# Optimization experiments

Measured on AMD Instinct MI355X. Metric: run time of the kernel, lower is better.

## Reference

```python
import jax, jax.numpy as jnp
import numpy as np

B, T, HID = 4, 2048, 2048
N_HEAD, N_KV, HD = 16, 2, 128
N_REP = N_HEAD // N_KV


def setup_inputs() -> dict:
    key = jax.random.key(0)
    ks = jax.random.split(key, 7)
    s = 0.02
    return {
        "x": jax.random.normal(ks[0], (B, T, HID), jnp.float32),
        "cos": jax.random.normal(ks[1], (T, 1, HD // 2), jnp.float32),
        "sin": jax.random.normal(ks[2], (T, 1, HD // 2), jnp.float32),
        "Wq": jax.random.normal(ks[3], (N_HEAD * HD, HID), jnp.float32) * s,
        "Wk": jax.random.normal(ks[4], (N_KV * HD, HID), jnp.float32) * s,
        "Wv": jax.random.normal(ks[5], (N_KV * HD, HID), jnp.float32) * s,
        "Wo": jax.random.normal(ks[6], (HID, HID), jnp.float32) * s,
    }


def _rope(x, cos, sin):
    # x: (B, T, H, HD); cos/sin: (T, 1, HD//2) broadcast over B and H
    x_r = x[..., 0::2]
    x_i = x[..., 1::2]
    out_r = x_r * cos - x_i * sin
    out_i = x_r * sin + x_i * cos
    return jnp.stack([out_r, out_i], axis=-1).reshape(x.shape)


def _rms_norm(x):
    eps = jnp.finfo(x.dtype).eps
    var = jnp.mean(jnp.square(x), axis=-1, keepdims=True)
    return x * jax.lax.rsqrt(var + eps)


def reference(x, cos, sin, Wq, Wk, Wv, Wo):
    b, t, _ = x.shape
    q = (x @ Wq.T).reshape(b, t, N_HEAD, HD)
    k = (x @ Wk.T).reshape(b, t, N_KV, HD)
    v = (x @ Wv.T).reshape(b, t, N_KV, HD)
    q = _rms_norm(_rope(q, cos, sin))
    k = _rms_norm(_rope(k, cos, sin))
    # GQA without materializing repeated K/V: group q heads per kv head
    # q: (b, t, n_kv, n_rep, hd) -> (b, n_kv, n_rep, t, hd)
    q = q.reshape(b, t, N_KV, N_REP, HD).transpose(0, 2, 3, 1, 4)
    k = k.transpose(0, 2, 1, 3)  # (b, n_kv, t, hd)
    v = v.transpose(0, 2, 1, 3)
    scale = 1.0 / jnp.sqrt(jnp.asarray(HD, x.dtype))
    scores = jnp.einsum("bgrtd,bgsd->bgrts", q, k) * scale
    causal = jnp.tril(jnp.ones((t, t), dtype=bool))
    scores = jnp.where(causal, scores, jnp.asarray(-jnp.inf, scores.dtype))
    attn = jax.nn.softmax(scores, axis=-1)
    y = jnp.einsum("bgrts,bgsd->bgrtd", attn, v)
    # (b, n_kv, n_rep, t, hd) -> (b, t, n_head*hd)
    y = y.transpose(0, 3, 1, 2, 4).reshape(b, t, N_HEAD * HD)
    return y @ Wo.T
```

## Files before the change

### kernel.cpp

```cpp
#include <hip/hip_runtime.h>

#define B_    4
#define T_    2048
#define HID_  2048
#define NH_   16
#define NKV_  2
#define HD_   128
#define M_    (B_ * T_)
#define NQKV_ 2560

typedef __bf16 bf16x8 __attribute__((ext_vector_type(8)));
typedef float  f32x4  __attribute__((ext_vector_type(4)));

#define AS1 __attribute__((address_space(1)))
#define AS3 __attribute__((address_space(3)))

#if __has_builtin(__builtin_amdgcn_exp2f)
#define EXP2(x) __builtin_amdgcn_exp2f(x)
#else
#define EXP2(x) exp2f(x)
#endif

__device__ __forceinline__ void load_lds16(const void* g, void* l) {
  __builtin_amdgcn_global_load_lds((const AS1 unsigned int*)g,
                                   (AS3 unsigned int*)l, 16, 0, 0);
}

__device__ __forceinline__ unsigned short f2bf(float x) {
  union { float f; unsigned u; } a; a.f = x;
  unsigned r = a.u + 0x7fffu + ((a.u >> 16) & 1u);
  return (unsigned short)(r >> 16);
}
__device__ __forceinline__ float bf2f(unsigned h) {
  union { unsigned u; float f; } a; a.u = h << 16;
  return a.f;
}
__device__ __forceinline__ unsigned pk_rtz(float lo, float hi) {
  union { float f; unsigned u; } a, b; a.f = lo; b.f = hi;
  return (a.u >> 16) | (b.u & 0xffff0000u);
}

__global__ __launch_bounds__(256) void cast_bf16(const float* __restrict__ in,
                                                 unsigned short* __restrict__ out,
                                                 int n4) {
  int i = blockIdx.x * 256 + threadIdx.x;
  if (i >= n4) return;
  float4 v = ((const float4*)in)[i];
  ushort4 o;
  o.x = f2bf(v.x); o.y = f2bf(v.y); o.z = f2bf(v.z); o.w = f2bf(v.w);
  ((ushort4*)out)[i] = o;
}

__global__ __launch_bounds__(256) void cast_w(const float* __restrict__ Wq,
                                              const float* __restrict__ Wk,
                                              const float* __restrict__ Wv,
                                              unsigned short* __restrict__ out) {
  int i = blockIdx.x * 256 + threadIdx.x;
  const float* src; int j;
  if (i < 1048576)      { src = Wq; j = i; }
  else if (i < 1179648) { src = Wk; j = i - 1048576; }
  else                  { src = Wv; j = i - 1179648; }
  float4 v = ((const float4*)src)[j];
  ushort4 o;
  o.x = f2bf(v.x); o.y = f2bf(v.y); o.z = f2bf(v.z); o.w = f2bf(v.w);
  ((ushort4*)out)[i] = o;
}

template <int OUT_BF16>
__global__ __launch_bounds__(256) void gemm_bt(const unsigned short* __restrict__ A,
                                               const unsigned short* __restrict__ Bm,
                                               void* __restrict__ C,
                                               int M, int N, int K) {
  __shared__ __align__(16) unsigned short As[128 * 32];
  __shared__ __align__(16) unsigned short Bs[128 * 32];
  const int tid = threadIdx.x;
  const int w = tid >> 6, lane = tid & 63;
  const int m0 = blockIdx.y << 7, n0 = blockIdx.x << 7;
  const int c = lane & 15, grp = lane >> 4;
  const int lr = lane >> 2;
  const int su = (((lane & 3) ^ ((lr >> 1) & 3)) << 3);
  const int sw = (c >> 1) & 3;
  const int wm = (w & 1) << 6, wn = (w >> 1) << 6;
  f32x4 acc[4][4] = {};
  for (int k0 = 0; k0 < K; k0 += 32) {
    __syncthreads();
    {
      int r0 = w << 4;
      load_lds16(A + (size_t)(m0 + r0 + lr) * K + k0 + su, &As[r0 * 32]);
      load_lds16(A + (size_t)(m0 + 64 + r0 + lr) * K + k0 + su, &As[(64 + r0) * 32]);
      load_lds16(Bm + (size_t)(n0 + r0 + lr) * K + k0 + su, &Bs[r0 * 32]);
      load_lds16(Bm + (size_t)(n0 + 64 + r0 + lr) * K + k0 + su, &Bs[(64 + r0) * 32]);
    }
    __syncthreads();
    bf16x8 af[4], bf[4];
#pragma unroll
    for (int i = 0; i < 4; i++)
      af[i] = *(const bf16x8*)&As[(wm + i * 16 + c) * 32 + ((grp ^ sw) << 3)];
#pragma unroll
    for (int j = 0; j < 4; j++)
      bf[j] = *(const bf16x8*)&Bs[(wn + j * 16 + c) * 32 + ((grp ^ sw) << 3)];
#pragma unroll
    for (int i = 0; i < 4; i++)
#pragma unroll
      for (int j = 0; j < 4; j++)
        acc[i][j] = __builtin_amdgcn_mfma_f32_16x16x32_bf16(af[i], bf[j], acc[i][j], 0, 0, 0);
  }
#pragma unroll
  for (int i = 0; i < 4; i++)
#pragma unroll
    for (int j = 0; j < 4; j++)
#pragma unroll
      for (int r = 0; r < 4; r++) {
        int row = m0 + wm + i * 16 + grp * 4 + r;
        int col = n0 + wn + j * 16 + c;
        float v = acc[i][j][r];
        if (OUT_BF16) ((unsigned short*)C)[(size_t)row * N + col] = f2bf(v);
        else          ((float*)C)[(size_t)row * N + col] = v;
      }
}

__global__ __launch_bounds__(256) void rope_norm(const unsigned short* __restrict__ qkv,
                                                 const float* __restrict__ cosb,
                                                 const float* __restrict__ sinb,
                                                 unsigned short* __restrict__ qo,
                                                 unsigned short* __restrict__ ko,
                                                 unsigned short* __restrict__ vo) {
  const int m = blockIdx.x;
  const int b = m >> 11, t = m & 2047;
  const int w = threadIdx.x >> 6, lane = threadIdx.x & 63;
  const float cv = cosb[t * 64 + lane], sv = sinb[t * 64 + lane];
  const unsigned short* row = qkv + (size_t)m * NQKV_;
  const float QSCL = 0.08838834764831845f * 1.4426950408889634f;
  for (int hh = w; hh < 20; hh += 4) {
    if (hh < 18) {
      const int col0 = (hh < 16) ? hh * 128 : 2048 + (hh - 16) * 128;
      unsigned pr = *(const unsigned*)(row + col0 + 2 * lane);
      float xr = bf2f(pr & 0xffffu), xi = bf2f(pr >> 16);
      float orr = xr * cv - xi * sv;
      float oi  = xr * sv + xi * cv;
      float ss = orr * orr + oi * oi;
#pragma unroll
      for (int off = 1; off < 64; off <<= 1) ss += __shfl_xor(ss, off);
      float scl = rsqrtf(ss * (1.0f / 128.0f) + 1.1920929e-07f);
      if (hh < 16) {
        float s2 = scl * QSCL;
        unsigned out = (unsigned)f2bf(orr * s2) | ((unsigned)f2bf(oi * s2) << 16);
        *(unsigned*)(qo + (((size_t)(b * NH_ + hh)) * T_ + t) * HD_ + 2 * lane) = out;
      } else {
        unsigned out = (unsigned)f2bf(orr * scl) | ((unsigned)f2bf(oi * scl) << 16);
        *(unsigned*)(ko + (((size_t)(b * NKV_ + (hh - 16))) * T_ + t) * HD_ + 2 * lane) = out;
      }
    } else {
      const int gg = hh - 18;
      unsigned pr = *(const unsigned*)(row + 2304 + gg * 128 + 2 * lane);
      *(unsigned*)(vo + (((size_t)(b * NKV_ + gg)) * T_ + t) * HD_ + 2 * lane) = pr;
    }
  }
}

__global__ __launch_bounds__(256) void transpose_v(const unsigned short* __restrict__ v,
                                                   unsigned short* __restrict__ vt) {
  __shared__ unsigned short tile[64][65];
  const int bg = blockIdx.z;
  const int t0 = blockIdx.x << 6, h0 = blockIdx.y << 6;
  const unsigned short* src = v + (size_t)bg * T_ * HD_;
  unsigned short* dst = vt + (size_t)bg * T_ * HD_;
  const int tid = threadIdx.x;
  const int rr = tid >> 4, cc = (tid & 15) << 2;
  const int u = (cc >> 2) & 7;
  const int cp = (cc & 32) + 16 * (u & 1) + 4 * ((u >> 1) & 3);
#pragma unroll
  for (int it = 0; it < 4; it++) {
    int r = rr + it * 16;
    ushort4 d = *(const ushort4*)(src + (size_t)(t0 + r) * HD_ + h0 + cc);
    tile[r][cc + 0] = d.x; tile[r][cc + 1] = d.y;
    tile[r][cc + 2] = d.z; tile[r][cc + 3] = d.w;
  }
  __syncthreads();
#pragma unroll
  for (int it = 0; it < 4; it++) {
    int r = rr + it * 16;
    ushort4 d;
    d.x = tile[cp + 0][r]; d.y = tile[cp + 1][r];
    d.z = tile[cp + 2][r]; d.w = tile[cp + 3][r];
    *(ushort4*)(dst + (size_t)(h0 + r) * T_ + t0 + cc) = d;
  }
}

__global__ __launch_bounds__(256, 2) void flash_attn(const unsigned short* __restrict__ q,
                                                     const unsigned short* __restrict__ k,
                                                     const unsigned short* __restrict__ vt,
                                                     unsigned short* __restrict__ y) {
  __shared__ __align__(16) unsigned short Kb[2][8192];
  __shared__ __align__(16) unsigned short Vb[2][8192];
  const int tid = threadIdx.x;
  const int w = tid >> 6, lane = tid & 63;
  const int c = lane & 15, grp = lane >> 4;
  const int lr = lane >> 2;
  const int sw = (c >> 1) & 3;
  const int su = (((lane & 3) ^ ((lr >> 1) & 3)) << 3);
  const int t0 = (15 - (int)blockIdx.x) << 7;
  const int t0w = t0 + w * 32;
  const int hq = blockIdx.y, b = blockIdx.z, g = hq >> 3;
  const unsigned short* qbase = q + (((size_t)(b * NH_ + hq)) * T_ + t0) * HD_;
  const unsigned short* kbase = k + ((size_t)(b * NKV_ + g)) * T_ * HD_;
  const unsigned short* vtbase = vt + ((size_t)(b * NKV_ + g)) * HD_ * T_;

  bf16x8 qf[2][4];
#pragma unroll
  for (int ti = 0; ti < 2; ti++)
#pragma unroll
    for (int ks = 0; ks < 4; ks++)
      qf[ti][ks] = *(const bf16x8*)(qbase + (size_t)(w * 32 + ti * 16 + c) * HD_ + ks * 32 + grp * 8);

  f32x4 oacc[2][8] = {};
  float mrun[2], lrun[2];
  mrun[0] = mrun[1] = -__builtin_inff();
  lrun[0] = lrun[1] = 0.f;

  auto stage = [&](int s0, int bb) {
    const unsigned short* kp = kbase + (size_t)(s0 + w * 16 + lr) * HD_ + su;
#pragma unroll
    for (int dc = 0; dc < 4; dc++)
      load_lds16(kp + dc * 32, &Kb[bb][dc * 2048 + (w * 16) * 32]);
    const unsigned short* vp = vtbase + s0 + su;
#pragma unroll
    for (int ks = 0; ks < 2; ks++)
#pragma unroll
      for (int jj = 0; jj < 2; jj++)
        load_lds16(vp + (size_t)(w * 32 + jj * 16 + lr) * T_ + ks * 32,
                   &Vb[bb][ks * 4096 + (w * 32 + jj * 16) * 32]);
  };

  const int nch = (t0 >> 6) + 2;
  stage(0, 0);
  __syncthreads();
  for (int ic = 0; ic < nch; ic++) {
    const int s0 = ic << 6, bb = ic & 1;
    if (ic + 1 < nch) stage((ic + 1) << 6, bb ^ 1);
    if (s0 <= t0w + 31) {
      const unsigned short* Kc = Kb[bb];
      const unsigned short* Vc = Vb[bb];
      f32x4 st[2][4] = {};
#pragma unroll
      for (int s = 0; s < 4; s++)
#pragma unroll
        for (int kvt = 0; kvt < 4; kvt++) {
          bf16x8 ak = *(const bf16x8*)&Kc[s * 2048 + (kvt * 16 + c) * 32 + ((grp ^ sw) << 3)];
          st[0][kvt] = __builtin_amdgcn_mfma_f32_16x16x32_bf16(ak, qf[0][s], st[0][kvt], 0, 0, 0);
          st[1][kvt] = __builtin_amdgcn_mfma_f32_16x16x32_bf16(ak, qf[1][s], st[1][kvt], 0, 0, 0);
        }
      if (s0 + 63 > t0w) {
#pragma unroll
        for (int ti = 0; ti < 2; ti++)
#pragma unroll
          for (int kvt = 0; kvt < 4; kvt++)
#pragma unroll
            for (int r = 0; r < 4; r++) {
              int kv = s0 + kvt * 16 + grp * 4 + r;
              int qq = t0w + ti * 16 + c;
              if (kv > qq) st[ti][kvt][r] = -__builtin_inff();
            }
      }
      unsigned pkv[2][4][2];
#pragma unroll
      for (int ti = 0; ti < 2; ti++) {
        float rm = st[ti][0][0];
#pragma unroll
        for (int kvt = 0; kvt < 4; kvt++)
#pragma unroll
          for (int r = 0; r < 4; r++) rm = fmaxf(rm, st[ti][kvt][r]);
        rm = fmaxf(rm, __shfl_xor(rm, 16));
        rm = fmaxf(rm, __shfl_xor(rm, 32));
        float mnew = fmaxf(mrun[ti], rm);
        float alpha = EXP2(mrun[ti] - mnew);
        mrun[ti] = mnew;
        float rs = 0.f;
#pragma unroll
        for (int kvt = 0; kvt < 4; kvt++) {
          float p0 = EXP2(st[ti][kvt][0] - mnew);
          float p1 = EXP2(st[ti][kvt][1] - mnew);
          float p2 = EXP2(st[ti][kvt][2] - mnew);
          float p3 = EXP2(st[ti][kvt][3] - mnew);
          rs += (p0 + p1) + (p2 + p3);
          pkv[ti][kvt][0] = pk_rtz(p0, p1);
          pkv[ti][kvt][1] = pk_rtz(p2, p3);
        }
        rs += __shfl_xor(rs, 16);
        rs += __shfl_xor(rs, 32);
        lrun[ti] = lrun[ti] * alpha + rs;
#pragma unroll
        for (int hj = 0; hj < 8; hj++)
#pragma unroll
          for (int r = 0; r < 4; r++) oacc[ti][hj][r] *= alpha;
      }
#pragma unroll
      for (int s = 0; s < 2; s++) {
        union { int4 i; bf16x8 v; } pf0, pf1;
        pf0.i = make_int4(pkv[0][2 * s][0], pkv[0][2 * s][1], pkv[0][2 * s + 1][0], pkv[0][2 * s + 1][1]);
        pf1.i = make_int4(pkv[1][2 * s][0], pkv[1][2 * s][1], pkv[1][2 * s + 1][0], pkv[1][2 * s + 1][1]);
#pragma unroll
        for (int hj = 0; hj < 8; hj++) {
          union { int4 i; bf16x8 v; } av;
          av.i = *(const int4*)&Vc[s * 4096 + (hj * 16 + c) * 32 + ((grp ^ sw) << 3)];
          oacc[0][hj] = __builtin_amdgcn_mfma_f32_16x16x32_bf16(av.v, pf0.v, oacc[0][hj], 0, 0, 0);
          oacc[1][hj] = __builtin_amdgcn_mfma_f32_16x16x32_bf16(av.v, pf1.v, oacc[1][hj], 0, 0, 0);
        }
      }
    }
    __syncthreads();
  }

#pragma unroll
  for (int ti = 0; ti < 2; ti++) {
    float inv = 1.f / lrun[ti];
    int trow = t0 + w * 32 + ti * 16 + c;
#pragma unroll
    for (int hj = 0; hj < 8; hj++) {
      ushort4 o;
      o.x = f2bf(oacc[ti][hj][0] * inv);
      o.y = f2bf(oacc[ti][hj][1] * inv);
      o.z = f2bf(oacc[ti][hj][2] * inv);
      o.w = f2bf(oacc[ti][hj][3] * inv);
      *(ushort4*)&y[((size_t)(b * T_ + trow)) * HID_ + hq * HD_ + hj * 16 + grp * 4] = o;
    }
  }
}

extern "C" void kernel_launch(void* const* d_in, const int* in_sizes, int n_in,
                              void* d_out, int out_size, void* d_ws, size_t ws_size,
                              hipStream_t stream) {
  const float* x    = (const float*)d_in[0];
  const float* cosb = (const float*)d_in[1];
  const float* sinb = (const float*)d_in[2];
  const float* Wq   = (const float*)d_in[3];
  const float* Wk   = (const float*)d_in[4];
  const float* Wv   = (const float*)d_in[5];
  const float* Wo   = (const float*)d_in[6];
  float* out = (float*)d_out;

  char* ws = (char*)d_ws;
  size_t off = 0;
  auto take = [&](size_t elems) {
    unsigned short* p = (unsigned short*)(ws + off);
    off += ((elems * 2 + 255) & ~(size_t)255);
    return p;
  };
  unsigned short* xb   = take((size_t)M_ * HID_);
  unsigned short* wqkv = take((size_t)NQKV_ * HID_);
  unsigned short* wob  = take((size_t)HID_ * HID_);
  unsigned short* qkv  = take((size_t)M_ * NQKV_);
  unsigned short* qb   = take((size_t)B_ * NH_ * T_ * HD_);
  unsigned short* kb   = take((size_t)B_ * NKV_ * T_ * HD_);
  unsigned short* vb   = take((size_t)B_ * NKV_ * T_ * HD_);
  unsigned short* vtb  = take((size_t)B_ * NKV_ * T_ * HD_);
  unsigned short* yb   = take((size_t)M_ * HID_);
  (void)ws_size; (void)in_sizes; (void)n_in; (void)out_size;

  cast_bf16<<<16384, 256, 0, stream>>>(x, xb, 4194304);
  cast_w<<<5120, 256, 0, stream>>>(Wq, Wk, Wv, wqkv);
  cast_bf16<<<4096, 256, 0, stream>>>(Wo, wob, 1048576);

  gemm_bt<1><<<dim3(20, 64), 256, 0, stream>>>(xb, wqkv, qkv, M_, NQKV_, HID_);
  rope_norm<<<8192, 256, 0, stream>>>(qkv, cosb, sinb, qb, kb, vb);
  transpose_v<<<dim3(32, 2, 8), 256, 0, stream>>>(vb, vtb);
  flash_attn<<<dim3(16, 16, 4), 256, 0, stream>>>(qb, kb, vtb, yb);
  gemm_bt<0><<<dim3(16, 64), 256, 0, stream>>>(yb, wob, out, M_, HID_, HID_);
}
```

Measured before the change: 549.8 us.

## Pair light and heavy causal query tiles in 512-thread flash attention blocks

Flash attention now launches 512-thread blocks of 8 waves. The first four waves take 32-row query slices from the start of the sequence and the last four take mirrored slices from the end, so every block does about the same causal work. K/V staging is shared across the 8 waves, each issuing fewer LDS loads. This targets load imbalance and tail effects across blocks, at the cost of early-finishing waves idling through the shared chunk loop and changed occupancy from the new launch bounds.

```diff
diff --git a/kernel.cpp b/kernel.cpp
--- a/kernel.cpp
+++ b/kernel.cpp
@@ -187,7 +187,7 @@
   }
 }
 
-__global__ __launch_bounds__(256, 2) void flash_attn(const unsigned short* __restrict__ q,
+__global__ __launch_bounds__(512, 4) void flash_attn(const unsigned short* __restrict__ q,
                                                      const unsigned short* __restrict__ k,
                                                      const unsigned short* __restrict__ vt,
                                                      unsigned short* __restrict__ y) {
@@ -199,10 +199,11 @@
   const int lr = lane >> 2;
   const int sw = (c >> 1) & 3;
   const int su = (((lane & 3) ^ ((lr >> 1) & 3)) << 3);
-  const int t0 = (15 - (int)blockIdx.x) << 7;
-  const int t0w = t0 + w * 32;
+  const int j = blockIdx.x;
+  const int sigma = (w < 4) ? (4 * j + w) : (60 - 4 * j + (w - 4));
+  const int qs = sigma << 5;
   const int hq = blockIdx.y, b = blockIdx.z, g = hq >> 3;
-  const unsigned short* qbase = q + (((size_t)(b * NH_ + hq)) * T_ + t0) * HD_;
+  const unsigned short* qbase = q + (((size_t)(b * NH_ + hq)) * T_ + qs) * HD_;
   const unsigned short* kbase = k + ((size_t)(b * NKV_ + g)) * T_ * HD_;
   const unsigned short* vtbase = vt + ((size_t)(b * NKV_ + g)) * HD_ * T_;
 
@@ -211,34 +212,33 @@
   for (int ti = 0; ti < 2; ti++)
 #pragma unroll
     for (int ks = 0; ks < 4; ks++)
-      qf[ti][ks] = *(const bf16x8*)(qbase + (size_t)(w * 32 + ti * 16 + c) * HD_ + ks * 32 + grp * 8);
+      qf[ti][ks] = *(const bf16x8*)(qbase + (size_t)(ti * 16 + c) * HD_ + ks * 32 + grp * 8);
 
   f32x4 oacc[2][8] = {};
   float mrun[2], lrun[2];
   mrun[0] = mrun[1] = -__builtin_inff();
   lrun[0] = lrun[1] = 0.f;
 
+  const int kdc = w >> 1, krb = (w & 1) << 5;
+  const int vks = (w >> 2) & 1, vrb = (w & 3) << 5;
   auto stage = [&](int s0, int bb) {
-    const unsigned short* kp = kbase + (size_t)(s0 + w * 16 + lr) * HD_ + su;
-#pragma unroll
-    for (int dc = 0; dc < 4; dc++)
-      load_lds16(kp + dc * 32, &Kb[bb][dc * 2048 + (w * 16) * 32]);
-    const unsigned short* vp = vtbase + s0 + su;
-#pragma unroll
-    for (int ks = 0; ks < 2; ks++)
-#pragma unroll
-      for (int jj = 0; jj < 2; jj++)
-        load_lds16(vp + (size_t)(w * 32 + jj * 16 + lr) * T_ + ks * 32,
-                   &Vb[bb][ks * 4096 + (w * 32 + jj * 16) * 32]);
+    load_lds16(kbase + (size_t)(s0 + krb + lr) * HD_ + kdc * 32 + su,
+               &Kb[bb][kdc * 2048 + krb * 32]);
+    load_lds16(kbase + (size_t)(s0 + krb + 16 + lr) * HD_ + kdc * 32 + su,
+               &Kb[bb][kdc * 2048 + (krb + 16) * 32]);
+    load_lds16(vtbase + (size_t)(vrb + lr) * T_ + s0 + vks * 32 + su,
+               &Vb[bb][vks * 4096 + vrb * 32]);
+    load_lds16(vtbase + (size_t)(vrb + 16 + lr) * T_ + s0 + vks * 32 + su,
+               &Vb[bb][vks * 4096 + (vrb + 16) * 32]);
   };
 
-  const int nch = (t0 >> 6) + 2;
+  const int nch = 32 - 2 * j;
   stage(0, 0);
   __syncthreads();
   for (int ic = 0; ic < nch; ic++) {
     const int s0 = ic << 6, bb = ic & 1;
     if (ic + 1 < nch) stage((ic + 1) << 6, bb ^ 1);
-    if (s0 <= t0w + 31) {
+    if (s0 <= qs + 31) {
       const unsigned short* Kc = Kb[bb];
       const unsigned short* Vc = Vb[bb];
       f32x4 st[2][4] = {};
@@ -250,7 +250,7 @@
           st[0][kvt] = __builtin_amdgcn_mfma_f32_16x16x32_bf16(ak, qf[0][s], st[0][kvt], 0, 0, 0);
           st[1][kvt] = __builtin_amdgcn_mfma_f32_16x16x32_bf16(ak, qf[1][s], st[1][kvt], 0, 0, 0);
         }
-      if (s0 + 63 > t0w) {
+      if (s0 + 63 > qs) {
 #pragma unroll
         for (int ti = 0; ti < 2; ti++)
 #pragma unroll
@@ -258,7 +258,7 @@
 #pragma unroll
             for (int r = 0; r < 4; r++) {
               int kv = s0 + kvt * 16 + grp * 4 + r;
-              int qq = t0w + ti * 16 + c;
+              int qq = qs + ti * 16 + c;
               if (kv > qq) st[ti][kvt][r] = -__builtin_inff();
             }
       }
@@ -314,7 +314,7 @@
 #pragma unroll
   for (int ti = 0; ti < 2; ti++) {
     float inv = 1.f / lrun[ti];
-    int trow = t0 + w * 32 + ti * 16 + c;
+    int trow = qs + ti * 16 + c;
 #pragma unroll
     for (int hj = 0; hj < 8; hj++) {
       ushort4 o;
@@ -364,6 +364,6 @@
   gemm_bt<1><<<dim3(20, 64), 256, 0, stream>>>(xb, wqkv, qkv, M_, NQKV_, HID_);
   rope_norm<<<8192, 256, 0, stream>>>(qkv, cosb, sinb, qb, kb, vb);
   transpose_v<<<dim3(32, 2, 8), 256, 0, stream>>>(vb, vtb);
-  flash_attn<<<dim3(16, 16, 4), 256, 0, stream>>>(qb, kb, vtb, yb);
+  flash_attn<<<dim3(8, 16, 4), 512, 0, stream>>>(qb, kb, vtb, yb);
   gemm_bt<0><<<dim3(16, 64), 256, 0, stream>>>(yb, wob, out, M_, HID_, HID_);
 }
```

Measured after the change: 641.4 us. +16.7%, slower.
